# Optimization experiments

Hardware: AMD Instinct MI355X
Metric: run time of the kernel (lower is better)

## Reference

```python
import jax, jax.numpy as jnp
import numpy as np

B, T, ENC, DEC, A = 64, 2048, 1024, 1024, 512


def setup_inputs() -> dict:
    key = jax.random.key(0)
    k1, k2, k3, k4, k5 = jax.random.split(key, 5)
    return {
        "h_j": jax.random.normal(k1, (B, T, ENC), dtype=jnp.float32),
        "s_t": jax.random.normal(k2, (B, DEC), dtype=jnp.float32),
        "U_w": jax.random.normal(k3, (ENC, A), dtype=jnp.float32) * (ENC ** -0.5),
        "W_w": jax.random.normal(k4, (DEC, A), dtype=jnp.float32) * (DEC ** -0.5),
        "V_w": jax.random.normal(k5, (A, 1), dtype=jnp.float32) * (A ** -0.5),
    }


def reference(h_j, s_t, U_w, W_w, V_w):
    # f1: [B, T, A] ; f2: [B, 1, A]
    f1 = jnp.einsum("bte,ea->bta", h_j, U_w)
    f2 = (s_t @ W_w)[:, None, :]
    # additive score e_t: [B, T, 1]
    e_t = jnp.tanh(f1 + f2) @ V_w
    a_t = jax.nn.softmax(e_t, axis=1)            # softmax over sequence axis
    c_t = jnp.sum(a_t * h_j, axis=1, keepdims=True)  # [B, 1, ENC]
    return (c_t, a_t)
```

## Files before the change

kernel.cpp:

```cpp
#include <hip/hip_runtime.h>
#include <hip/hip_bf16.h>
#include <stdint.h>

#define B_   64
#define T_   2048
#define ENC_ 1024
#define DEC_ 1024
#define A_   512
#define M_   (B_ * T_)

#define BM 128
#define BN 256
#define BK 64

typedef __bf16 bf16x8 __attribute__((ext_vector_type(8)));
typedef float  f32x4  __attribute__((ext_vector_type(4)));
typedef unsigned short u16;
typedef u16 u16x8 __attribute__((ext_vector_type(8)));

__device__ __forceinline__ float fast_tanh(float x) {
    float ax = fabsf(x);
    float e  = __expf(-2.0f * ax);
    float t  = (1.0f - e) / (1.0f + e);
    return copysignf(t, x);
}

__global__ __launch_bounds__(256) void k_transpose_U(
        const float* __restrict__ U, u16* __restrict__ Ut) {
    int idx = blockIdx.x * 256 + threadIdx.x;
    if (idx >= ENC_ * A_) return;
    int k = idx / A_, n = idx % A_;
    __bf16 v = (__bf16)U[idx];
    Ut[n * ENC_ + k] = *(u16*)&v;
}

__global__ __launch_bounds__(256) void k_f2(
        const float* __restrict__ s, const float* __restrict__ W,
        float* __restrict__ f2) {
    int b = blockIdx.x;
    int a0 = threadIdx.x;
    const float* srow = s + (size_t)b * DEC_;
    float acc0 = 0.f, acc1 = 0.f;
    for (int e = 0; e < DEC_; ++e) {
        float sv = srow[e];
        acc0 = fmaf(sv, W[(size_t)e * A_ + a0],       acc0);
        acc1 = fmaf(sv, W[(size_t)e * A_ + a0 + 256], acc1);
    }
    f2[(size_t)b * A_ + a0]       = acc0;
    f2[(size_t)b * A_ + a0 + 256] = acc1;
}

__global__ __launch_bounds__(512, 4) void k_gemm_e(
        const float* __restrict__ h, const u16* __restrict__ Ut,
        const float* __restrict__ f2, const float* __restrict__ V,
        float* __restrict__ e_part) {
    __shared__ u16 Alds[BM * BK];
    __shared__ u16 Blds[BN * BK];

    const int tid  = threadIdx.x;
    const int lane = tid & 63;
    const int wid  = tid >> 6;
    const int wr   = wid >> 2;
    const int wc   = wid & 3;
    const int lr   = lane & 15;
    const int g    = lane >> 4;
    const int sw   = (lr & 7) << 3;

    const int d    = blockIdx.x;
    const int xcd  = d & 7;
    const int s    = d >> 3;
    const int m    = s & 1;
    const int pair = xcd * 128 + (s >> 1);
    const int brow = pair * BM;
    const int bcol = m * BN;
    const int b    = brow / T_;

    f32x4 acc[4][4] = {};

    for (int kt = 0; kt < ENC_ / BK; ++kt) {
        const int k0 = kt * BK;

#pragma unroll
        for (int it = 0; it < 4; ++it) {
            int G  = it * 512 + tid;
            int n  = G >> 3;
            int kc = ((G & 7) ^ (n & 7)) << 3;
            const u16* src = Ut + (size_t)(bcol + n) * ENC_ + k0 + kc;
            u16* dst = &Blds[(size_t)(it * 512 + wid * 64) * 8];
            __builtin_amdgcn_global_load_lds(
                (const __attribute__((address_space(1))) void*)src,
                (__attribute__((address_space(3))) void*)dst, 16, 0, 0);
        }

#pragma unroll
        for (int it = 0; it < 2; ++it) {
            int flat = (it * 512 + tid) * 8;
            int r = flat >> 6, c = flat & 63;
            const float* srcA = h + (size_t)(brow + r) * ENC_ + k0 + c;
            f32x4 v0 = *(const f32x4*)srcA;
            f32x4 v1 = *(const f32x4*)(srcA + 4);
            u16x8 w;
#pragma unroll
            for (int j = 0; j < 4; ++j) {
                __bf16 lo = (__bf16)v0[j], hi = (__bf16)v1[j];
                w[j]     = *(u16*)&lo;
                w[j + 4] = *(u16*)&hi;
            }
            *(u16x8*)&Alds[flat ^ ((r & 7) << 3)] = w;
        }
        __syncthreads();

#pragma unroll
        for (int kk = 0; kk < 2; ++kk) {
            bf16x8 af[4], bfr[4];
#pragma unroll
            for (int mf = 0; mf < 4; ++mf)
                af[mf] = *(const bf16x8*)&Alds[
                    (((wr * 64 + mf * 16 + lr) * 64) + kk * 32 + g * 8) ^ sw];
#pragma unroll
            for (int nf = 0; nf < 4; ++nf)
                bfr[nf] = *(const bf16x8*)&Blds[
                    (((wc * 64 + nf * 16 + lr) * 64) + kk * 32 + g * 8) ^ sw];
#pragma unroll
            for (int mf = 0; mf < 4; ++mf)
#pragma unroll
                for (int nf = 0; nf < 4; ++nf)
                    acc[mf][nf] = __builtin_amdgcn_mfma_f32_16x16x32_bf16(
                        af[mf], bfr[nf], acc[mf][nf], 0, 0, 0);
        }
        __syncthreads();
    }

    float vv[4], ff[4];
#pragma unroll
    for (int nf = 0; nf < 4; ++nf) {
        int n = bcol + wc * 64 + nf * 16 + lr;
        vv[nf] = V[n];
        ff[nf] = f2[(size_t)b * A_ + n];
    }
    const int p = m * 4 + wc;
    float* ep = e_part + (size_t)p * M_ + brow + wr * 64;
#pragma unroll
    for (int mf = 0; mf < 4; ++mf) {
        float sums[4];
#pragma unroll
        for (int i = 0; i < 4; ++i) {
            float sv = 0.f;
#pragma unroll
            for (int nf = 0; nf < 4; ++nf) {
                float x = acc[mf][nf][i] + ff[nf];
                sv = fmaf(fast_tanh(x), vv[nf], sv);
            }
#pragma unroll
            for (int mm = 1; mm < 16; mm <<= 1)
                sv += __shfl_xor(sv, mm, 64);
            sums[i] = sv;
        }
        if (lr == 0) {
#pragma unroll
            for (int i = 0; i < 4; ++i)
                ep[mf * 16 + g * 4 + i] = sums[i];
        }
    }
}

__global__ __launch_bounds__(256) void k_softmax(
        const float* __restrict__ e_part, float* __restrict__ a_out) {
    const int b = blockIdx.x, tid = threadIdx.x;
    const int lane = tid & 63, w = tid >> 6;
    __shared__ float red[4], red2[4];

    float ls[8];
    float lmax = -1e30f;
#pragma unroll
    for (int i = 0; i < 8; ++i) {
        size_t mm = (size_t)b * T_ + i * 256 + tid;
        float sv = 0.f;
#pragma unroll
        for (int p = 0; p < 8; ++p) sv += e_part[(size_t)p * M_ + mm];
        ls[i] = sv;
        lmax = fmaxf(lmax, sv);
    }
#pragma unroll
    for (int mm = 1; mm < 64; mm <<= 1) lmax = fmaxf(lmax, __shfl_xor(lmax, mm, 64));
    if (lane == 0) red[w] = lmax;
    __syncthreads();
    float bmax = fmaxf(fmaxf(red[0], red[1]), fmaxf(red[2], red[3]));

    float lsum = 0.f;
#pragma unroll
    for (int i = 0; i < 8; ++i) { ls[i] = __expf(ls[i] - bmax); lsum += ls[i]; }
#pragma unroll
    for (int mm = 1; mm < 64; mm <<= 1) lsum += __shfl_xor(lsum, mm, 64);
    if (lane == 0) red2[w] = lsum;
    __syncthreads();
    float inv = 1.0f / (red2[0] + red2[1] + red2[2] + red2[3]);

#pragma unroll
    for (int i = 0; i < 8; ++i)
        a_out[(size_t)b * T_ + i * 256 + tid] = ls[i] * inv;
}

__global__ __launch_bounds__(256) void k_ctx_part(
        const float* __restrict__ h, const float* __restrict__ a,
        float* __restrict__ c_part) {
    const int b = blockIdx.x, tc = blockIdx.y, tid = threadIdx.x;
    __shared__ float alds[128];
    if (tid < 128)
        alds[tid] = a[(size_t)b * T_ + tc * 128 + tid];
    __syncthreads();

    float4 acc = {0.f, 0.f, 0.f, 0.f};
    const float* hb = h + ((size_t)b * T_ + (size_t)tc * 128) * ENC_ + tid * 4;
    for (int t = 0; t < 128; ++t) {
        float av = alds[t];
        float4 hv = *(const float4*)(hb + (size_t)t * ENC_);
        acc.x = fmaf(av, hv.x, acc.x);
        acc.y = fmaf(av, hv.y, acc.y);
        acc.z = fmaf(av, hv.z, acc.z);
        acc.w = fmaf(av, hv.w, acc.w);
    }
    *(float4*)&c_part[((size_t)(tc * 64 + b)) * ENC_ + tid * 4] = acc;
}

__global__ __launch_bounds__(256) void k_ctx_final(
        const float* __restrict__ c_part, float* __restrict__ c_out) {
    int idx = blockIdx.x * 256 + threadIdx.x;
    int off = idx * 4;
    float4 sv = {0.f, 0.f, 0.f, 0.f};
#pragma unroll
    for (int tc = 0; tc < 16; ++tc) {
        float4 v = *(const float4*)&c_part[(size_t)tc * 64 * 1024 + off];
        sv.x += v.x; sv.y += v.y; sv.z += v.z; sv.w += v.w;
    }
    *(float4*)&c_out[off] = sv;
}

extern "C" void kernel_launch(void* const* d_in, const int* in_sizes, int n_in,
                              void* d_out, int out_size, void* d_ws, size_t ws_size,
                              hipStream_t stream) {
    const float* h = (const float*)d_in[0];
    const float* s = (const float*)d_in[1];
    const float* U = (const float*)d_in[2];
    const float* W = (const float*)d_in[3];
    const float* V = (const float*)d_in[4];

    float* out   = (float*)d_out;
    float* c_out = out;
    float* a_out = out + 64 * 1024;

    char* ws = (char*)d_ws;
    u16*   Ut     = (u16*)ws;
    float* f2     = (float*)(ws + (1 << 20));
    float* e_part = (float*)(ws + (1 << 20) + (128 << 10));
    float* c_part = e_part;

    k_transpose_U<<<2048, 256, 0, stream>>>(U, Ut);
    k_f2<<<64, 256, 0, stream>>>(s, W, f2);

    k_gemm_e<<<2048, 512, 0, stream>>>(h, Ut, f2, V, e_part);

    k_softmax<<<64, 256, 0, stream>>>(e_part, a_out);

    dim3 gc(64, 16);
    k_ctx_part<<<gc, 256, 0, stream>>>(h, a_out, c_part);
    k_ctx_final<<<64, 256, 0, stream>>>(c_part, c_out);
}
```

Measured before the change: 346.1 us.

## Double-buffer A tile in LDS and read B fragments directly from global

```diff
diff --git a/kernel.cpp b/kernel.cpp
--- a/kernel.cpp
+++ b/kernel.cpp
@@ -54,8 +54,7 @@
         const float* __restrict__ h, const u16* __restrict__ Ut,
         const float* __restrict__ f2, const float* __restrict__ V,
         float* __restrict__ e_part) {
-    __shared__ u16 Alds[BM * BK];
-    __shared__ u16 Blds[BN * BK];
+    __shared__ u16 Alds[2][BM * BK];
 
     const int tid  = threadIdx.x;
     const int lane = tid & 63;
@@ -75,52 +74,56 @@
     const int bcol = m * BN;
     const int b    = brow / T_;
 
+    const u16* bw = Ut + (size_t)(bcol + wc * 64 + lr) * ENC_ + g * 8;
+
     f32x4 acc[4][4] = {};
 
-    for (int kt = 0; kt < ENC_ / BK; ++kt) {
-        const int k0 = kt * BK;
-
-#pragma unroll
-        for (int it = 0; it < 4; ++it) {
-            int G  = it * 512 + tid;
-            int n  = G >> 3;
-            int kc = ((G & 7) ^ (n & 7)) << 3;
-            const u16* src = Ut + (size_t)(bcol + n) * ENC_ + k0 + kc;
-            u16* dst = &Blds[(size_t)(it * 512 + wid * 64) * 8];
-            __builtin_amdgcn_global_load_lds(
-                (const __attribute__((address_space(1))) void*)src,
-                (__attribute__((address_space(3))) void*)dst, 16, 0, 0);
-        }
-
+    f32x4 ar[4];
+    auto loadA = [&](int kt) {
+        int flat0 = tid * 8;
+        int r = flat0 >> 6, c = flat0 & 63;
+        const float* srcA = h + (size_t)(brow + r) * ENC_ + kt * BK + c;
+        ar[0] = *(const f32x4*)srcA;
+        ar[1] = *(const f32x4*)(srcA + 4);
+        const float* srcB = srcA + (size_t)64 * ENC_;
+        ar[2] = *(const f32x4*)srcB;
+        ar[3] = *(const f32x4*)(srcB + 4);
+    };
+    auto writeA = [&](int buf) {
 #pragma unroll
         for (int it = 0; it < 2; ++it) {
             int flat = (it * 512 + tid) * 8;
-            int r = flat >> 6, c = flat & 63;
-            const float* srcA = h + (size_t)(brow + r) * ENC_ + k0 + c;
-            f32x4 v0 = *(const f32x4*)srcA;
-            f32x4 v1 = *(const f32x4*)(srcA + 4);
+            int r = flat >> 6;
             u16x8 w;
 #pragma unroll
             for (int j = 0; j < 4; ++j) {
-                __bf16 lo = (__bf16)v0[j], hi = (__bf16)v1[j];
+                __bf16 lo = (__bf16)ar[it * 2][j], hi = (__bf16)ar[it * 2 + 1][j];
                 w[j]     = *(u16*)&lo;
                 w[j + 4] = *(u16*)&hi;
             }
-            *(u16x8*)&Alds[flat ^ ((r & 7) << 3)] = w;
-        }
-        __syncthreads();
-
+            *(u16x8*)&Alds[buf][flat ^ ((r & 7) << 3)] = w;
+        }
+    };
+
+    loadA(0);
+    writeA(0);
+    __syncthreads();
+
+    for (int kt = 0; kt < ENC_ / BK; ++kt) {
+        const int cur = kt & 1;
+        if (kt + 1 < ENC_ / BK) loadA(kt + 1);
+        const int k0 = kt * BK;
 #pragma unroll
         for (int kk = 0; kk < 2; ++kk) {
             bf16x8 af[4], bfr[4];
 #pragma unroll
+            for (int nf = 0; nf < 4; ++nf)
+                bfr[nf] = *(const bf16x8*)(bw + (size_t)nf * 16 * ENC_
+                                              + k0 + kk * 32);
+#pragma unroll
             for (int mf = 0; mf < 4; ++mf)
-                af[mf] = *(const bf16x8*)&Alds[
+                af[mf] = *(const bf16x8*)&Alds[cur][
                     (((wr * 64 + mf * 16 + lr) * 64) + kk * 32 + g * 8) ^ sw];
-#pragma unroll
-            for (int nf = 0; nf < 4; ++nf)
-                bfr[nf] = *(const bf16x8*)&Blds[
-                    (((wc * 64 + nf * 16 + lr) * 64) + kk * 32 + g * 8) ^ sw];
 #pragma unroll
             for (int mf = 0; mf < 4; ++mf)
 #pragma unroll
@@ -128,6 +131,7 @@
                     acc[mf][nf] = __builtin_amdgcn_mfma_f32_16x16x32_bf16(
                         af[mf], bfr[nf], acc[mf][nf], 0, 0, 0);
         }
+        if (kt + 1 < ENC_ / BK) writeA(cur ^ 1);
         __syncthreads();
     }
 
```

Result: slower. 495.7 us (+43.2%).

## Stream fp32 activation tile into LDS asynchronously and convert to bf16 at fragment load

Applied to the files above, without the earlier changes.

```diff
diff --git a/kernel.cpp b/kernel.cpp
--- a/kernel.cpp
+++ b/kernel.cpp
@@ -16,7 +16,6 @@
 typedef __bf16 bf16x8 __attribute__((ext_vector_type(8)));
 typedef float  f32x4  __attribute__((ext_vector_type(4)));
 typedef unsigned short u16;
-typedef u16 u16x8 __attribute__((ext_vector_type(8)));
 
 __device__ __forceinline__ float fast_tanh(float x) {
     float ax = fabsf(x);
@@ -54,8 +53,8 @@
         const float* __restrict__ h, const u16* __restrict__ Ut,
         const float* __restrict__ f2, const float* __restrict__ V,
         float* __restrict__ e_part) {
-    __shared__ u16 Alds[BM * BK];
-    __shared__ u16 Blds[BN * BK];
+    __shared__ float Af[BM * BK];
+    __shared__ u16   Blds[BN * BK];
 
     const int tid  = threadIdx.x;
     const int lane = tid & 63;
@@ -64,7 +63,8 @@
     const int wc   = wid & 3;
     const int lr   = lane & 15;
     const int g    = lane >> 4;
-    const int sw   = (lr & 7) << 3;
+    const int swb  = (lr & 7) << 3;
+    const int swa  = lr & 7;
 
     const int d    = blockIdx.x;
     const int xcd  = d & 7;
@@ -80,6 +80,17 @@
     for (int kt = 0; kt < ENC_ / BK; ++kt) {
         const int k0 = kt * BK;
 
+#pragma unroll
+        for (int it = 0; it < 4; ++it) {
+            int G   = it * 512 + tid;
+            int row = G >> 4, sl = G & 15;
+            const float* src = h + (size_t)(brow + row) * ENC_ + k0
+                                 + ((sl ^ (row & 7)) << 2);
+            float* dst = Af + (size_t)(it * 512 + wid * 64) * 4;
+            __builtin_amdgcn_global_load_lds(
+                (const __attribute__((address_space(1))) void*)src,
+                (__attribute__((address_space(3))) void*)dst, 16, 0, 0);
+        }
 #pragma unroll
         for (int it = 0; it < 4; ++it) {
             int G  = it * 512 + tid;
@@ -91,36 +102,27 @@
                 (const __attribute__((address_space(1))) void*)src,
                 (__attribute__((address_space(3))) void*)dst, 16, 0, 0);
         }
-
-#pragma unroll
-        for (int it = 0; it < 2; ++it) {
-            int flat = (it * 512 + tid) * 8;
-            int r = flat >> 6, c = flat & 63;
-            const float* srcA = h + (size_t)(brow + r) * ENC_ + k0 + c;
-            f32x4 v0 = *(const f32x4*)srcA;
-            f32x4 v1 = *(const f32x4*)(srcA + 4);
-            u16x8 w;
-#pragma unroll
-            for (int j = 0; j < 4; ++j) {
-                __bf16 lo = (__bf16)v0[j], hi = (__bf16)v1[j];
-                w[j]     = *(u16*)&lo;
-                w[j + 4] = *(u16*)&hi;
-            }
-            *(u16x8*)&Alds[flat ^ ((r & 7) << 3)] = w;
-        }
         __syncthreads();
 
 #pragma unroll
         for (int kk = 0; kk < 2; ++kk) {
             bf16x8 af[4], bfr[4];
 #pragma unroll
-            for (int mf = 0; mf < 4; ++mf)
-                af[mf] = *(const bf16x8*)&Alds[
-                    (((wr * 64 + mf * 16 + lr) * 64) + kk * 32 + g * 8) ^ sw];
+            for (int mf = 0; mf < 4; ++mf) {
+                int row  = wr * 64 + mf * 16 + lr;
+                int base = row * 64 + kk * 32;
+                f32x4 f0 = *(const f32x4*)&Af[base + (((2 * g)     ^ swa) << 2)];
+                f32x4 f1 = *(const f32x4*)&Af[base + (((2 * g + 1) ^ swa) << 2)];
+#pragma unroll
+                for (int j = 0; j < 4; ++j) {
+                    af[mf][j]     = (__bf16)f0[j];
+                    af[mf][j + 4] = (__bf16)f1[j];
+                }
+            }
 #pragma unroll
             for (int nf = 0; nf < 4; ++nf)
                 bfr[nf] = *(const bf16x8*)&Blds[
-                    (((wc * 64 + nf * 16 + lr) * 64) + kk * 32 + g * 8) ^ sw];
+                    (((wc * 64 + nf * 16 + lr) * 64) + kk * 32 + g * 8) ^ swb];
 #pragma unroll
             for (int mf = 0; mf < 4; ++mf)
 #pragma unroll
```

New measurement: 360.9 us. 1.04x slower.

## Double-buffer LDS and software-pipeline A/B loads in the score GEMM

Applied to the files above, without the earlier changes.

```diff
diff --git a/kernel.cpp b/kernel.cpp
--- a/kernel.cpp
+++ b/kernel.cpp
@@ -10,8 +10,9 @@
 #define M_   (B_ * T_)
 
 #define BM 128
-#define BN 256
-#define BK 64
+#define BN 128
+#define BK 32
+#define NT (ENC_ / BK)
 
 typedef __bf16 bf16x8 __attribute__((ext_vector_type(8)));
 typedef float  f32x4  __attribute__((ext_vector_type(4)));
@@ -50,85 +51,113 @@
     f2[(size_t)b * A_ + a0 + 256] = acc1;
 }
 
-__global__ __launch_bounds__(512, 4) void k_gemm_e(
+__global__ __launch_bounds__(256, 8) void k_gemm_e(
         const float* __restrict__ h, const u16* __restrict__ Ut,
         const float* __restrict__ f2, const float* __restrict__ V,
         float* __restrict__ e_part) {
-    __shared__ u16 Alds[BM * BK];
-    __shared__ u16 Blds[BN * BK];
+    __shared__ u16 Ab[2][BM * BK];
+    __shared__ u16 Bb[2][BN * BK];
 
     const int tid  = threadIdx.x;
     const int lane = tid & 63;
     const int wid  = tid >> 6;
-    const int wr   = wid >> 2;
-    const int wc   = wid & 3;
+    const int wr   = wid >> 1;
+    const int wc   = wid & 1;
     const int lr   = lane & 15;
     const int g    = lane >> 4;
-    const int sw   = (lr & 7) << 3;
+    const int swr  = (lr & 3) << 3;
 
     const int d    = blockIdx.x;
     const int xcd  = d & 7;
     const int s    = d >> 3;
-    const int m    = s & 1;
-    const int pair = xcd * 128 + (s >> 1);
-    const int brow = pair * BM;
+    const int m    = s & 3;
+    const int pr   = xcd * 128 + (s >> 2);
+    const int brow = pr * BM;
     const int bcol = m * BN;
     const int b    = brow / T_;
 
     f32x4 acc[4][4] = {};
-
-    for (int kt = 0; kt < ENC_ / BK; ++kt) {
-        const int k0 = kt * BK;
-
-#pragma unroll
-        for (int it = 0; it < 4; ++it) {
-            int G  = it * 512 + tid;
-            int n  = G >> 3;
-            int kc = ((G & 7) ^ (n & 7)) << 3;
-            const u16* src = Ut + (size_t)(bcol + n) * ENC_ + k0 + kc;
-            u16* dst = &Blds[(size_t)(it * 512 + wid * 64) * 8];
+    f32x4 ar[4];
+
+    const int arow = tid >> 1;
+    const int acol = (tid & 1) << 4;
+    auto loadA = [&](int kt) {
+        const float* src = h + (size_t)(brow + arow) * ENC_ + kt * BK + acol;
+        ar[0] = *(const f32x4*)src;       ar[1] = *(const f32x4*)(src + 4);
+        ar[2] = *(const f32x4*)(src + 8); ar[3] = *(const f32x4*)(src + 12);
+    };
+    auto writeA = [&](u16* A) {
+        int cb = (tid & 1) << 1;
+        u16x8 w0, w1;
+#pragma unroll
+        for (int j = 0; j < 4; ++j) {
+            __bf16 a0 = (__bf16)ar[0][j], a1 = (__bf16)ar[1][j];
+            __bf16 a2 = (__bf16)ar[2][j], a3 = (__bf16)ar[3][j];
+            w0[j] = *(u16*)&a0; w0[j + 4] = *(u16*)&a1;
+            w1[j] = *(u16*)&a2; w1[j + 4] = *(u16*)&a3;
+        }
+        *(u16x8*)&A[arow * 32 + ((cb     ^ (arow & 3)) << 3)] = w0;
+        *(u16x8*)&A[arow * 32 + ((cb + 1) ^ (arow & 3) ) * 8] = w1;
+    };
+    auto stageB = [&](u16* Bd, int kt) {
+#pragma unroll
+        for (int it = 0; it < 2; ++it) {
+            int G  = it * 256 + tid;
+            int n  = G >> 2;
+            int kc = ((G & 3) ^ (n & 3)) << 3;
+            const u16* src = Ut + (size_t)(bcol + n) * ENC_ + kt * BK + kc;
+            u16* dst = &Bd[(size_t)(it * 256 + wid * 64) * 8];
             __builtin_amdgcn_global_load_lds(
                 (const __attribute__((address_space(1))) void*)src,
                 (__attribute__((address_space(3))) void*)dst, 16, 0, 0);
         }
-
-#pragma unroll
-        for (int it = 0; it < 2; ++it) {
-            int flat = (it * 512 + tid) * 8;
-            int r = flat >> 6, c = flat & 63;
-            const float* srcA = h + (size_t)(brow + r) * ENC_ + k0 + c;
-            f32x4 v0 = *(const f32x4*)srcA;
-            f32x4 v1 = *(const f32x4*)(srcA + 4);
-            u16x8 w;
-#pragma unroll
-            for (int j = 0; j < 4; ++j) {
-                __bf16 lo = (__bf16)v0[j], hi = (__bf16)v1[j];
-                w[j]     = *(u16*)&lo;
-                w[j + 4] = *(u16*)&hi;
+    };
+    auto compute = [&](const u16* A, const u16* Bc) {
+        bf16x8 af[4], bfr[4];
+#pragma unroll
+        for (int mf = 0; mf < 4; ++mf) {
+            int row = wr * 64 + mf * 16 + lr;
+            af[mf] = *(const bf16x8*)&A[(row * 32 + g * 8) ^ swr];
+        }
+#pragma unroll
+        for (int nf = 0; nf < 4; ++nf) {
+            int n = wc * 64 + nf * 16 + lr;
+            bfr[nf] = *(const bf16x8*)&Bc[(n * 32 + g * 8) ^ swr];
+        }
+#pragma unroll
+        for (int mf = 0; mf < 4; ++mf)
+#pragma unroll
+            for (int nf = 0; nf < 4; ++nf)
+                acc[mf][nf] = __builtin_amdgcn_mfma_f32_16x16x32_bf16(
+                    af[mf], bfr[nf], acc[mf][nf], 0, 0, 0);
+    };
+
+#define BAR()   __builtin_amdgcn_s_barrier()
+#define LGKM0() asm volatile("s_waitcnt lgkmcnt(0)" ::: "memory")
+#define VMC4()  asm volatile("s_waitcnt vmcnt(4)" ::: "memory")
+#define VMC0()  asm volatile("s_waitcnt vmcnt(0)" ::: "memory")
+
+    loadA(0);
+    stageB(Bb[0], 0);
+    writeA(Ab[0]);
+    loadA(1);
+    VMC4();
+    LGKM0(); BAR();
+
+    for (int t = 0; t < NT; ++t) {
+        const int cur = t & 1;
+        if (t + 1 < NT) stageB(Bb[cur ^ 1], t + 1);
+        compute(Ab[cur], Bb[cur]);
+        if (t + 1 < NT) {
+            writeA(Ab[cur ^ 1]);
+            if (t + 2 < NT) {
+                loadA(t + 2);
+                VMC4();
+            } else {
+                VMC0();
             }
-            *(u16x8*)&Alds[flat ^ ((r & 7) << 3)] = w;
-        }
-        __syncthreads();
-
-#pragma unroll
-        for (int kk = 0; kk < 2; ++kk) {
-            bf16x8 af[4], bfr[4];
-#pragma unroll
-            for (int mf = 0; mf < 4; ++mf)
-                af[mf] = *(const bf16x8*)&Alds[
-                    (((wr * 64 + mf * 16 + lr) * 64) + kk * 32 + g * 8) ^ sw];
-#pragma unroll
-            for (int nf = 0; nf < 4; ++nf)
-                bfr[nf] = *(const bf16x8*)&Blds[
-                    (((wc * 64 + nf * 16 + lr) * 64) + kk * 32 + g * 8) ^ sw];
-#pragma unroll
-            for (int mf = 0; mf < 4; ++mf)
-#pragma unroll
-                for (int nf = 0; nf < 4; ++nf)
-                    acc[mf][nf] = __builtin_amdgcn_mfma_f32_16x16x32_bf16(
-                        af[mf], bfr[nf], acc[mf][nf], 0, 0, 0);
-        }
-        __syncthreads();
+            LGKM0(); BAR();
+        }
     }
 
     float vv[4], ff[4];
@@ -138,7 +167,7 @@
         vv[nf] = V[n];
         ff[nf] = f2[(size_t)b * A_ + n];
     }
-    const int p = m * 4 + wc;
+    const int p = m * 2 + wc;
     float* ep = e_part + (size_t)p * M_ + brow + wr * 64;
 #pragma unroll
     for (int mf = 0; mf < 4; ++mf) {
@@ -162,6 +191,10 @@
                 ep[mf * 16 + g * 4 + i] = sums[i];
         }
     }
+#undef BAR
+#undef LGKM0
+#undef VMC4
+#undef VMC0
 }
 
 __global__ __launch_bounds__(256) void k_softmax(
@@ -258,7 +291,7 @@
     k_transpose_U<<<2048, 256, 0, stream>>>(U, Ut);
     k_f2<<<64, 256, 0, stream>>>(s, W, f2);
 
-    k_gemm_e<<<2048, 512, 0, stream>>>(h, Ut, f2, V, e_part);
+    k_gemm_e<<<4096, 256, 0, stream>>>(h, Ut, f2, V, e_part);
 
     k_softmax<<<64, 256, 0, stream>>>(e_part, a_out);
 
```

After: 521.5 us. +50.7%, slower.
